# Kernel tuning notes

Hardware: AMD Instinct MI355X
Metric: run time of the kernel (lower is better)

The kernel has to match this reference:

```python
import jax, jax.numpy as jnp
import numpy as np

B, T, E = 2, 2048, 1024
H, D = 16, 64
FF = 4096
EPS = 1e-5


def _layer_norm(x, g, b):
    m = jnp.mean(x, axis=-1, keepdims=True)
    v = jnp.mean(jnp.square(x - m), axis=-1, keepdims=True)
    return (x - m) * jax.lax.rsqrt(v + EPS) * g + b


def setup_inputs() -> dict:
    key = jax.random.key(0)
    ks = jax.random.split(key, 8)
    s = lambda fan_in: 1.0 / np.sqrt(fan_in)
    return {
        "src": jax.random.normal(ks[0], (B, T, E), jnp.float32),
        "Wq": jax.random.normal(ks[1], (E, E), jnp.float32) * s(E),
        "Wk": jax.random.normal(ks[2], (E, E), jnp.float32) * s(E),
        "Wv": jax.random.normal(ks[3], (E, E), jnp.float32) * s(E),
        "Wo": jax.random.normal(ks[4], (E, E), jnp.float32) * s(E),
        "W1": jax.random.normal(ks[5], (2 * FF, E), jnp.float32) * s(E),
        "b1": jnp.zeros((2 * FF,), jnp.float32),
        "W2": jax.random.normal(ks[6], (E, FF), jnp.float32) * s(FF),
        "b2": jnp.zeros((E,), jnp.float32),
        "ln1_w": jnp.ones((E,), jnp.float32),
        "ln1_b": jnp.zeros((E,), jnp.float32),
        "ln2_w": jnp.ones((E,), jnp.float32),
        "ln2_b": jnp.zeros((E,), jnp.float32),
    }


def reference(src, Wq, Wk, Wv, Wo, W1, b1, W2, b2, ln1_w, ln1_b, ln2_w, ln2_b):
    # --- pre-norm self-attention block ---
    h = _layer_norm(src, ln1_w, ln1_b)                       # [B,T,E]
    q = (h @ Wq.T).reshape(B, T, H, D)                       # [B,T,H,D]
    k = (h @ Wk.T).reshape(B, T, H, D)
    v = (h @ Wv.T).reshape(B, T, H, D)
    scores = jnp.einsum("bqhd,bkhd->bhqk", q, k) / np.sqrt(D)
    probs = jax.nn.softmax(scores, axis=-1)                  # [B,H,T,T]
    attn = jnp.einsum("bhqk,bkhd->bqhd", probs, v).reshape(B, T, E)
    x = src + attn @ Wo.T                                    # residual (dropout=0)
    # --- pre-norm GEGLU FFN block ---
    h2 = _layer_norm(x, ln2_w, ln2_b)
    u = h2 @ W1.T + b1                                       # [B,T,2*FF]
    a, gates = jnp.split(u, 2, axis=-1)
    f = a * jax.nn.gelu(gates, approximate=False)            # GEGLU (exact erf gelu)
    return x + (f @ W2.T + b2)
```

## Files before the change

kernel.cpp:

```cpp
#include <hip/hip_runtime.h>
#include <stdint.h>
#include <math.h>

#define DEVI __device__ __forceinline__

typedef __attribute__((ext_vector_type(8))) short sv8;
typedef __attribute__((ext_vector_type(4))) short sv4;
typedef __attribute__((ext_vector_type(4))) float fv4;

typedef __attribute__((address_space(1))) void av1_t;
typedef __attribute__((address_space(3))) void av3_t;

constexpr int Bb = 2, Tt = 2048, Ee = 1024, Hh = 16, Dd = 64, FFd = 4096;
constexpr int NN = Bb * Tt;
constexpr float EPSv = 1e-5f;

DEVI float b2f(unsigned short s) {
  union { unsigned u; float f; } v; v.u = ((unsigned)s) << 16; return v.f;
}
DEVI unsigned short f2b(float f) {
  union { float f; unsigned u; } v; v.f = f;
  return (unsigned short)((v.u + 0x7FFFu + ((v.u >> 16) & 1u)) >> 16);
}
DEVI unsigned short f2b_rtz(float f) {
  union { float f; unsigned u; } v; v.f = f;
  return (unsigned short)(v.u >> 16);
}

DEVI void load_lds16(const void* g, void* s) {
  __builtin_amdgcn_global_load_lds((av1_t*)(unsigned long long)g,
                                   (av3_t*)(unsigned)(unsigned long long)s,
                                   16, 0, 0);
}

__global__ __launch_bounds__(256) void cvt_kernel(const float* __restrict__ in,
                                                  unsigned short* __restrict__ out, int n,
                                                  float scale) {
  int i = (blockIdx.x * 256 + threadIdx.x) * 4;
  if (i >= n) return;
  float4 v = *(const float4*)(in + i);
  sv4 o;
  o[0] = (short)f2b(v.x * scale); o[1] = (short)f2b(v.y * scale);
  o[2] = (short)f2b(v.z * scale); o[3] = (short)f2b(v.w * scale);
  *(sv4*)(out + i) = o;
}

__global__ __launch_bounds__(256) void cvt_w1_kernel(const float* __restrict__ in,
                                                     unsigned short* __restrict__ out) {
  int i = (blockIdx.x * 256 + threadIdx.x) * 4;
  const int r = i >> 10, c = i & 1023;
  const int rp = (r < FFd) ? ((r >> 4) * 32 + (r & 15))
                           : (((r - FFd) >> 4) * 32 + 16 + (r & 15));
  float4 v = *(const float4*)(in + i);
  sv4 o;
  o[0] = (short)f2b(v.x); o[1] = (short)f2b(v.y);
  o[2] = (short)f2b(v.z); o[3] = (short)f2b(v.w);
  *(sv4*)(out + (size_t)rp * Ee + c) = o;
}

__global__ __launch_bounds__(256) void vt_kernel(const unsigned short* __restrict__ qkv,
                                                 unsigned short* __restrict__ vT) {
  const int bh = blockIdx.y;
  const int b = bh >> 4, h = bh & 15;
  const int tt = blockIdx.x * 64;
  const int tid = threadIdx.x;
  __shared__ unsigned short tile[64][65];
  const int tr = tid >> 2, tc4 = (tid & 3) * 16;
  const unsigned short* src = qkv + (size_t)(b * Tt + tt + tr) * (3 * Ee) + 2 * Ee + h * 64 + tc4;
  const sv8 a0 = *(const sv8*)src;
  const sv8 a1 = *(const sv8*)(src + 8);
#pragma unroll
  for (int j = 0; j < 8; ++j) { tile[tr][tc4 + j] = a0[j]; tile[tr][tc4 + 8 + j] = a1[j]; }
  __syncthreads();
  unsigned short* dst = vT + ((size_t)bh * 64 + tr) * Tt + tt + tc4;
  sv8 o0, o1;
#pragma unroll
  for (int j = 0; j < 8; ++j) { o0[j] = (short)tile[tc4 + j][tr]; o1[j] = (short)tile[tc4 + 8 + j][tr]; }
  *(sv8*)dst = o0;
  *(sv8*)(dst + 8) = o1;
}

__global__ __launch_bounds__(256) void ln_kernel(const float* __restrict__ x,
                                                 const float* __restrict__ g,
                                                 const float* __restrict__ b,
                                                 unsigned short* __restrict__ out) {
  const int row = blockIdx.x, tid = threadIdx.x;
  const float4 v = *(const float4*)(x + (size_t)row * Ee + tid * 4);
  float s = v.x + v.y + v.z + v.w;
  float ss = v.x * v.x + v.y * v.y + v.z * v.z + v.w * v.w;
#pragma unroll
  for (int off = 32; off; off >>= 1) { s += __shfl_down(s, off); ss += __shfl_down(ss, off); }
  __shared__ float red[16];
  const int w = tid >> 6, l = tid & 63;
  if (l == 0) { red[w] = s; red[8 + w] = ss; }
  __syncthreads();
  s = red[0] + red[1] + red[2] + red[3];
  ss = red[8] + red[9] + red[10] + red[11];
  const float mean = s * (1.f / Ee);
  const float rstd = rsqrtf(ss * (1.f / Ee) - mean * mean + EPSv);
  const float4 gv = *(const float4*)(g + tid * 4);
  const float4 bv = *(const float4*)(b + tid * 4);
  sv4 o;
  o[0] = (short)f2b((v.x - mean) * rstd * gv.x + bv.x);
  o[1] = (short)f2b((v.y - mean) * rstd * gv.y + bv.y);
  o[2] = (short)f2b((v.z - mean) * rstd * gv.z + bv.z);
  o[3] = (short)f2b((v.w - mean) * rstd * gv.w + bv.w);
  *(sv4*)(out + (size_t)row * Ee + tid * 4) = o;
}

template <int OUTF32, int HASBIAS, int BN, int GEGLU>
__global__ __launch_bounds__(256) void gemm_bt(const unsigned short* __restrict__ A,
                                               const unsigned short* __restrict__ Bw,
                                               void* __restrict__ Cout,
                                               const float* __restrict__ bias,
                                               const float* __restrict__ res,
                                               int M, int K) {
  constexpr int NI = BN / 32;
  __shared__ unsigned short lA[2][128 * 32];
  __shared__ unsigned short lB[2][BN * 32];
  const int tid = threadIdx.x;
  const int l = tid & 63, w = tid >> 6;
  const int wr = w >> 1, wc = w & 1;
  const int rowbase = blockIdx.y * 128, colbase = blockIdx.x * BN;

  const fv4 zero4 = {0.f, 0.f, 0.f, 0.f};
  fv4 acc[4][NI];
#pragma unroll
  for (int i = 0; i < 4; ++i)
#pragma unroll
    for (int j = 0; j < NI; ++j) acc[i][j] = zero4;

  const int c0 = tid, c1 = tid + 256;
  const int sw0 = ((c0 & 3) ^ ((c0 >> 3) & 3)) * 8;
  const int sw1 = ((c1 & 3) ^ ((c1 >> 3) & 3)) * 8;
  const unsigned short* Ag0 = A + (size_t)(rowbase + (c0 >> 2)) * K + sw0;
  const unsigned short* Ag1 = A + (size_t)(rowbase + (c1 >> 2)) * K + sw1;
  const unsigned short* Bg0 = Bw + (size_t)(colbase + (c0 >> 2)) * K + sw0;
  const unsigned short* Bg1 = Bw + (size_t)(colbase + ((BN == 128 ? c1 : c0) >> 2)) * K +
                              (BN == 128 ? sw1 : sw0);

  const int nk = K >> 5;

  load_lds16(Ag0, lA[0] + c0 * 8);
  load_lds16(Ag1, lA[0] + c1 * 8);
  load_lds16(Bg0, lB[0] + c0 * 8);
  if (BN == 128) load_lds16(Bg1, lB[0] + c1 * 8);
  Ag0 += 32; Ag1 += 32; Bg0 += 32; Bg1 += 32;
  __syncthreads();

  int cur = 0;
  for (int kt = 0; kt < nk; ++kt) {
    const int nx = cur ^ 1;
    if (kt + 1 < nk) {
      load_lds16(Ag0, lA[nx] + c0 * 8);
      load_lds16(Ag1, lA[nx] + c1 * 8);
      load_lds16(Bg0, lB[nx] + c0 * 8);
      if (BN == 128) load_lds16(Bg1, lB[nx] + c1 * 8);
      Ag0 += 32; Ag1 += 32; Bg0 += 32; Bg1 += 32;
    }
    sv8 af[4], bfr[NI];
#pragma unroll
    for (int i = 0; i < 4; ++i) {
      const int ra = wr * 64 + i * 16 + (l & 15);
      af[i] = *(const sv8*)(lA[cur] + ra * 32 + (((l >> 4) ^ ((ra >> 1) & 3)) * 8));
    }
#pragma unroll
    for (int i = 0; i < NI; ++i) {
      const int rb = wc * (BN / 2) + i * 16 + (l & 15);
      bfr[i] = *(const sv8*)(lB[cur] + rb * 32 + (((l >> 4) ^ ((rb >> 1) & 3)) * 8));
    }
    __builtin_amdgcn_s_setprio(1);
#pragma unroll
    for (int mi = 0; mi < 4; ++mi)
#pragma unroll
      for (int ni = 0; ni < NI; ++ni)
        acc[mi][ni] = __builtin_amdgcn_mfma_f32_16x16x32_bf16(af[mi], bfr[ni], acc[mi][ni], 0, 0, 0);
    __builtin_amdgcn_s_setprio(0);
    __syncthreads();
    cur = nx;
  }

  const int r0 = rowbase + wr * 64 + ((l >> 4) * 4);
  const int ccol = colbase + wc * (BN / 2) + (l & 15);
#pragma unroll
  for (int mi = 0; mi < 4; ++mi) {
#pragma unroll
    for (int j = 0; j < 4; ++j) {
      const size_t r = (size_t)(r0 + mi * 16 + j);
      if (GEGLU) {
#pragma unroll
        for (int p = 0; p < NI / 2; ++p) {
          const int ca = ccol + p * 32;
          const int ocol = ((ca >> 5) << 4) | (ca & 15);
          const float av = acc[mi][2 * p][j] + bias[ocol];
          const float gv = acc[mi][2 * p + 1][j] + bias[ocol + (M >> 1)];
          const float y = 0.7978845608028654f * (gv + 0.044715f * gv * gv * gv);
          const float e = exp2f(2.8853900817779268f * y);
          const float gel = gv * (1.f - 1.f / (e + 1.f));
          ((unsigned short*)Cout)[r * (size_t)(M >> 1) + ocol] = f2b(av * gel);
        }
      } else {
#pragma unroll
        for (int ni = 0; ni < NI; ++ni) {
          const int c = ccol + ni * 16;
          float vv = acc[mi][ni][j];
          if (HASBIAS) vv += bias[c];
          if (OUTF32) {
            ((float*)Cout)[r * M + c] = res[r * M + c] + vv;
          } else {
            ((unsigned short*)Cout)[r * M + c] = f2b(vv);
          }
        }
      }
    }
  }
}

__global__ __launch_bounds__(256) void attn_kernel(const unsigned short* __restrict__ Q,
                                                   const unsigned short* __restrict__ Kb,
                                                   const unsigned short* __restrict__ vT,
                                                   unsigned short* __restrict__ O,
                                                   int ld) {
  const int bidl = ((blockIdx.x & 7) << 7) + (blockIdx.x >> 3);
  const int bh = bidl >> 5;
  const int b = bh / Hh, h = bh % Hh;
  const int q0 = (bidl & 31) * 64;
  const int tid = threadIdx.x, l = tid & 63, w = tid >> 6;
  const size_t base = (size_t)b * Tt * ld + (size_t)h * Dd;
  const size_t baseO = (size_t)b * Tt * Ee + (size_t)h * Dd;
  const unsigned short* vTb = vT + (size_t)bh * 64 * Tt;

  __shared__ unsigned short Kt[2][64 * 64];
  __shared__ unsigned short Vt[2][64 * 64];
  __shared__ unsigned short Pt[4][16 * 64];

  sv8 qf0, qf1;
  {
    const unsigned short* qp = Q + base + (size_t)(q0 + w * 16 + (l & 15)) * ld + (l >> 4) * 8;
    qf0 = *(const sv8*)qp;
    qf1 = *(const sv8*)(qp + 32);
  }

  const fv4 zero4 = {0.f, 0.f, 0.f, 0.f};
  fv4 acc_o[4];
#pragma unroll
  for (int i = 0; i < 4; ++i) acc_o[i] = zero4;
  float Mx = -INFINITY;
  float Lp[4];
#pragma unroll
  for (int j = 0; j < 4; ++j) Lp[j] = 0.f;

  const int c0 = tid, c1 = tid + 256;
  const int r0c = c0 >> 3, xc0 = c0 & 7;
  const int r1c = c1 >> 3, xc1 = c1 & 7;

  load_lds16(Kb + base + (size_t)(r0c)*ld + (xc0 ^ (r0c & 7)) * 8, Kt[0] + c0 * 8);
  load_lds16(Kb + base + (size_t)(r1c)*ld + (xc1 ^ (r1c & 7)) * 8, Kt[0] + c1 * 8);
  load_lds16(vTb + (size_t)(r0c)*Tt + (xc0 ^ (r0c & 7)) * 8, Vt[0] + c0 * 8);
  load_lds16(vTb + (size_t)(r1c)*Tt + (xc1 ^ (r1c & 7)) * 8, Vt[0] + c1 * 8);
  __syncthreads();

  int cur = 0;
  for (int kt = 0; kt < Tt / 64; ++kt) {
    const int nx = cur ^ 1;
    if (kt + 1 < Tt / 64) {
      load_lds16(Kb + base + (size_t)((kt + 1) * 64 + r0c) * ld + (xc0 ^ (r0c & 7)) * 8, Kt[nx] + c0 * 8);
      load_lds16(Kb + base + (size_t)((kt + 1) * 64 + r1c) * ld + (xc1 ^ (r1c & 7)) * 8, Kt[nx] + c1 * 8);
      load_lds16(vTb + (size_t)(r0c)*Tt + (kt + 1) * 64 + (xc0 ^ (r0c & 7)) * 8, Vt[nx] + c0 * 8);
      load_lds16(vTb + (size_t)(r1c)*Tt + (kt + 1) * 64 + (xc1 ^ (r1c & 7)) * 8, Vt[nx] + c1 * 8);
    }

    fv4 s[4];
    __builtin_amdgcn_s_setprio(1);
#pragma unroll
    for (int ks = 0; ks < 4; ++ks) {
      const int row = ks * 16 + (l & 15);
      const sv8 kf0 = *(const sv8*)(Kt[cur] + row * 64 + (((l >> 4) ^ (row & 7)) * 8));
      const sv8 kf1 = *(const sv8*)(Kt[cur] + row * 64 + (((4 + (l >> 4)) ^ (row & 7)) * 8));
      fv4 t = zero4;
      t = __builtin_amdgcn_mfma_f32_16x16x32_bf16(qf0, kf0, t, 0, 0, 0);
      t = __builtin_amdgcn_mfma_f32_16x16x32_bf16(qf1, kf1, t, 0, 0, 0);
      s[ks] = t;
    }
    __builtin_amdgcn_s_setprio(0);

    float m01 = fmaxf(fmaxf(s[0][0], s[0][1]), fmaxf(s[0][2], s[0][3]));
    float m1 = fmaxf(fmaxf(s[1][0], s[1][1]), fmaxf(s[1][2], s[1][3]));
    float m2 = fmaxf(fmaxf(s[2][0], s[2][1]), fmaxf(s[2][2], s[2][3]));
    float m3 = fmaxf(fmaxf(s[3][0], s[3][1]), fmaxf(s[3][2], s[3][3]));
    float tm = fmaxf(fmaxf(m01, m1), fmaxf(m2, m3));
    if (__any(tm > Mx + 11.5f)) {
      float mt = tm;
#pragma unroll
      for (int off = 1; off < 16; off <<= 1) mt = fmaxf(mt, __shfl_xor(mt, off, 16));
      const float mnew = fmaxf(Mx, mt);
      const float alpha = exp2f(Mx - mnew);
      Mx = mnew;
#pragma unroll
      for (int j = 0; j < 4; ++j) {
        Lp[j] *= alpha;
#pragma unroll
        for (int dsb = 0; dsb < 4; ++dsb) acc_o[dsb][j] *= alpha;
      }
    }
#pragma unroll
    for (int ks = 0; ks < 4; ++ks)
#pragma unroll
      for (int j = 0; j < 4; ++j) {
        const float p = exp2f(s[ks][j] - Mx);
        s[ks][j] = p;
        Lp[j] += p;
      }
#pragma unroll
    for (int ks = 0; ks < 4; ++ks)
#pragma unroll
      for (int j = 0; j < 4; ++j) {
        const int q = (l >> 4) * 4 + j, k = ks * 16 + (l & 15);
        Pt[w][q * 64 + ((((k >> 3) ^ (q & 7)) & 7) * 8) + (k & 7)] = f2b_rtz(s[ks][j]);
      }
    asm volatile("s_waitcnt lgkmcnt(0)" ::: "memory");

    __builtin_amdgcn_s_setprio(1);
#pragma unroll
    for (int kcn = 0; kcn < 2; ++kcn) {
      const int qr = l & 15;
      const sv8 pf = *(const sv8*)(&Pt[w][qr * 64 + (((kcn * 4 + (l >> 4)) ^ (qr & 7)) * 8)]);
#pragma unroll
      for (int dsb = 0; dsb < 4; ++dsb) {
        const int row = dsb * 16 + (l & 15);
        const int chunk = kcn * 4 + (l >> 4);
        const sv8 vf = *(const sv8*)(Vt[cur] + row * 64 + ((chunk ^ (row & 7)) * 8));
        acc_o[dsb] = __builtin_amdgcn_mfma_f32_16x16x32_bf16(pf, vf, acc_o[dsb], 0, 0, 0);
      }
    }
    __builtin_amdgcn_s_setprio(0);

    __syncthreads();
    cur = nx;
  }

#pragma unroll
  for (int j = 0; j < 4; ++j) {
    float t = Lp[j];
#pragma unroll
    for (int off = 1; off < 16; off <<= 1) t += __shfl_xor(t, off, 16);
    const float inv = 1.f / t;
    unsigned short* op = O + baseO + (size_t)(q0 + w * 16 + (l >> 4) * 4 + j) * Ee;
#pragma unroll
    for (int dsb = 0; dsb < 4; ++dsb)
      op[dsb * 16 + (l & 15)] = f2b(acc_o[dsb][j] * inv);
  }
}

extern "C" void kernel_launch(void* const* d_in, const int* in_sizes, int n_in,
                              void* d_out, int out_size, void* d_ws, size_t ws_size,
                              hipStream_t stream) {
  (void)in_sizes; (void)n_in; (void)out_size; (void)ws_size;
  const float* src  = (const float*)d_in[0];
  const float* Wq   = (const float*)d_in[1];
  const float* Wk   = (const float*)d_in[2];
  const float* Wv   = (const float*)d_in[3];
  const float* Wo   = (const float*)d_in[4];
  const float* W1   = (const float*)d_in[5];
  const float* b1   = (const float*)d_in[6];
  const float* W2   = (const float*)d_in[7];
  const float* b2   = (const float*)d_in[8];
  const float* ln1w = (const float*)d_in[9];
  const float* ln1b = (const float*)d_in[10];
  const float* ln2w = (const float*)d_in[11];
  const float* ln2b = (const float*)d_in[12];
  float* out = (float*)d_out;

  char* ws = (char*)d_ws;
  size_t off = 0;
  auto alloc = [&](size_t bytes) { char* p = ws + off; off += bytes; return p; };
  unsigned short* wqkv = (unsigned short*)alloc((size_t)3 * Ee * Ee * 2);
  unsigned short* wo16 = (unsigned short*)alloc((size_t)Ee * Ee * 2);
  unsigned short* w116 = (unsigned short*)alloc((size_t)2 * FFd * Ee * 2);
  unsigned short* w216 = (unsigned short*)alloc((size_t)Ee * FFd * 2);
  unsigned short* h16  = (unsigned short*)alloc((size_t)NN * Ee * 2);
  unsigned short* qkv  = (unsigned short*)alloc((size_t)NN * 3 * Ee * 2);
  unsigned short* a16  = (unsigned short*)alloc((size_t)NN * Ee * 2);
  float* xbuf          = (float*)alloc((size_t)NN * Ee * 4);
  unsigned short* vT   = (unsigned short*)alloc((size_t)NN * Ee * 2);
  unsigned short* f16  = qkv;

  const float s2 = 0.125f * 1.4426950408889634f;

  dim3 blk(256);
  cvt_kernel<<<dim3(Ee * Ee / 1024), blk, 0, stream>>>(Wq, wqkv, Ee * Ee, s2);
  cvt_kernel<<<dim3(Ee * Ee / 1024), blk, 0, stream>>>(Wk, wqkv + Ee * Ee, Ee * Ee, 1.0f);
  cvt_kernel<<<dim3(Ee * Ee / 1024), blk, 0, stream>>>(Wv, wqkv + 2 * Ee * Ee, Ee * Ee, 1.0f);
  cvt_kernel<<<dim3(Ee * Ee / 1024), blk, 0, stream>>>(Wo, wo16, Ee * Ee, 1.0f);
  cvt_w1_kernel<<<dim3(2 * FFd * Ee / 1024), blk, 0, stream>>>(W1, w116);
  cvt_kernel<<<dim3(Ee * FFd / 1024), blk, 0, stream>>>(W2, w216, Ee * FFd, 1.0f);

  ln_kernel<<<dim3(NN), blk, 0, stream>>>(src, ln1w, ln1b, h16);

  gemm_bt<0, 0, 128, 0><<<dim3(3 * Ee / 128, NN / 128), blk, 0, stream>>>(h16, wqkv, qkv, nullptr, nullptr, 3 * Ee, Ee);

  vt_kernel<<<dim3(Tt / 64, Bb * Hh), blk, 0, stream>>>(qkv, vT);

  attn_kernel<<<dim3(1024), blk, 0, stream>>>(qkv, qkv + Ee, vT, a16, 3 * Ee);

  gemm_bt<1, 0, 64, 0><<<dim3(Ee / 64, NN / 128), blk, 0, stream>>>(a16, wo16, xbuf, nullptr, src, Ee, Ee);

  ln_kernel<<<dim3(NN), blk, 0, stream>>>(xbuf, ln2w, ln2b, h16);

  gemm_bt<0, 0, 128, 1><<<dim3(2 * FFd / 128, NN / 128), blk, 0, stream>>>(h16, w116, f16, b1, nullptr, 2 * FFd, Ee);

  gemm_bt<1, 1, 64, 0><<<dim3(Ee / 64, NN / 128), blk, 0, stream>>>(f16, w216, out, b2, xbuf, Ee, FFd);
}
```

Baseline: 320.0 us.

## Triple-buffer GEMM LDS tiles with partial vmcnt waits instead of full syncs

Moves the bf16 GEMM main loop from double to triple buffering in LDS, issuing global-to-LDS loads two k-tiles ahead. Explicit s_waitcnt vmcnt(N) plus a raw s_barrier replace __syncthreads, so only the oldest stage has to land before each iteration and more load latency is hidden behind MFMA work. LDS use grows by half, which can lower occupancy. The barrier sits after the reads of the current buffer, so the buffer being refilled at the top of the next iteration is no longer being read.

```diff
diff --git a/kernel.cpp b/kernel.cpp
--- a/kernel.cpp
+++ b/kernel.cpp
@@ -14,6 +14,8 @@
 constexpr int Bb = 2, Tt = 2048, Ee = 1024, Hh = 16, Dd = 64, FFd = 4096;
 constexpr int NN = Bb * Tt;
 constexpr float EPSv = 1e-5f;
+
+#define WAIT_VM(n) asm volatile("s_waitcnt vmcnt(" #n ")" ::: "memory")
 
 DEVI float b2f(unsigned short s) {
   union { unsigned u; float f; } v; v.u = ((unsigned)s) << 16; return v.f;
@@ -116,8 +118,8 @@
                                                const float* __restrict__ res,
                                                int M, int K) {
   constexpr int NI = BN / 32;
-  __shared__ unsigned short lA[2][128 * 32];
-  __shared__ unsigned short lB[2][BN * 32];
+  __shared__ unsigned short lA[3][128 * 32];
+  __shared__ unsigned short lB[3][BN * 32];
   const int tid = threadIdx.x;
   const int l = tid & 63, w = tid >> 6;
   const int wr = w >> 1, wc = w & 1;
@@ -141,23 +143,23 @@
 
   const int nk = K >> 5;
 
-  load_lds16(Ag0, lA[0] + c0 * 8);
-  load_lds16(Ag1, lA[0] + c1 * 8);
-  load_lds16(Bg0, lB[0] + c0 * 8);
-  if (BN == 128) load_lds16(Bg1, lB[0] + c1 * 8);
-  Ag0 += 32; Ag1 += 32; Bg0 += 32; Bg1 += 32;
-  __syncthreads();
+  auto stage = [&](int buf) {
+    load_lds16(Ag0, lA[buf] + c0 * 8);
+    load_lds16(Ag1, lA[buf] + c1 * 8);
+    load_lds16(Bg0, lB[buf] + c0 * 8);
+    if (BN == 128) load_lds16(Bg1, lB[buf] + c1 * 8);
+    Ag0 += 32; Ag1 += 32; Bg0 += 32; Bg1 += 32;
+  };
+
+  stage(0);
+  stage(1);
+  if constexpr (BN == 128) WAIT_VM(4); else WAIT_VM(3);
+  __builtin_amdgcn_s_barrier();
 
   int cur = 0;
-  for (int kt = 0; kt < nk; ++kt) {
-    const int nx = cur ^ 1;
-    if (kt + 1 < nk) {
-      load_lds16(Ag0, lA[nx] + c0 * 8);
-      load_lds16(Ag1, lA[nx] + c1 * 8);
-      load_lds16(Bg0, lB[nx] + c0 * 8);
-      if (BN == 128) load_lds16(Bg1, lB[nx] + c1 * 8);
-      Ag0 += 32; Ag1 += 32; Bg0 += 32; Bg1 += 32;
-    }
+  for (int t = 0; t < nk; ++t) {
+    const int pf = (cur + 2 >= 3) ? cur - 1 : cur + 2;
+    if (t + 2 < nk) stage(pf);
     sv8 af[4], bfr[NI];
 #pragma unroll
     for (int i = 0; i < 4; ++i) {
@@ -176,8 +178,14 @@
       for (int ni = 0; ni < NI; ++ni)
         acc[mi][ni] = __builtin_amdgcn_mfma_f32_16x16x32_bf16(af[mi], bfr[ni], acc[mi][ni], 0, 0, 0);
     __builtin_amdgcn_s_setprio(0);
-    __syncthreads();
-    cur = nx;
+    if (t + 2 < nk) {
+      if constexpr (BN == 128) WAIT_VM(4); else WAIT_VM(3);
+      __builtin_amdgcn_s_barrier();
+    } else if (t + 1 < nk) {
+      WAIT_VM(0);
+      __builtin_amdgcn_s_barrier();
+    }
+    cur = (cur + 1 >= 3) ? 0 : cur + 1;
   }
 
   const int r0 = rowbase + wr * 64 + ((l >> 4) * 4);
```

After: 315.3 us. Within noise of the previous version (-1.5%).
